# Optimization experiments

Hardware: AMD Instinct MI355X
Metric: run time of the kernel (lower is better)

The kernel has to match this reference:

```python
import jax, jax.numpy as jnp
import numpy as np

K = 5  # filter_size (matches init_kwargs)


def _adaptive_pool_matrix(size: int, k: int) -> jnp.ndarray:
    """Row-stochastic [k, size] matrix replicating torch adaptive_avg_pool1d bins."""
    P = np.zeros((k, size), np.float32)
    for i in range(k):
        s = (i * size) // k
        e = -((-(i + 1) * size) // k)  # ceil((i+1)*size/k)
        P[i, s:e] = 1.0 / (e - s)
    return jnp.asarray(P)


def setup_inputs() -> dict:
    key = jax.random.key(0)
    k1, k2, k3 = jax.random.split(key, 3)
    B, Cin, Cout, H, W = 8, 32, 32, 256, 256
    x = jax.random.normal(k1, (B, Cin, H, W), jnp.float32)
    conv_w = jax.random.normal(k2, (Cout, Cin), jnp.float32) * (1.0 / np.sqrt(Cin))
    conv_b = jax.random.normal(k3, (Cout,), jnp.float32) * 0.01
    return {"x": x, "conv_w": conv_w, "conv_b": conv_b}


def reference(x, conv_w, conv_b):
    B, Cin, H, W = x.shape
    # 1x1 conv == channel-mixing einsum
    feat = jnp.einsum('bihw,oi->bohw', x, conv_w) + conv_b[None, :, None, None]
    C = feat.shape[1]
    # adaptive_avg_pool2d(feat, K) via static pooling matrices -> per-(b,c) KxK filter
    Ph = _adaptive_pool_matrix(H, K)
    Pw = _adaptive_pool_matrix(W, K)
    filt = jnp.einsum('kh,bchw,lw->bckl', Ph, feat, Pw)  # [B, C, K, K]
    # pad per original intent ('same' output), then grouped conv with groups=B*C
    pad = (K - 1) // 2
    if (K - 1) % 2 == 0:
        p = ((pad, pad), (pad, pad))
    else:
        p = ((pad + 1, pad), (pad + 1, pad))
    inp = feat.reshape(1, B * C, H, W)
    w = filt.reshape(B * C, 1, K, K)
    out = jax.lax.conv_general_dilated(
        inp, w, window_strides=(1, 1), padding=p,
        dimension_numbers=('NCHW', 'OIHW', 'NCHW'),
        feature_group_count=B * C)
    return out.reshape(B, C, H, W)
```

## Files before the change

### kernel.cpp

```cpp
#include <hip/hip_runtime.h>
#include <hip/hip_bf16.h>


#define CIN 32
#define COUT 32
#define HW 256
#define PLANE (HW * HW)
#define BATCH 8
#define KF 5

__global__ __launch_bounds__(256) void conv1x1_kernel(const float* __restrict__ x,
                                                      const float* __restrict__ Wm,
                                                      const float* __restrict__ bias,
                                                      float* __restrict__ feat) {
    int b  = blockIdx.x >> 7;
    int hp = blockIdx.x & 127;
    int h0 = hp * 2;
    int w  = threadIdx.x;

    const float* xb = x + (size_t)b * CIN * PLANE + h0 * HW + w;
    float xv0[CIN], xv1[CIN];
#pragma unroll
    for (int i = 0; i < CIN; ++i) {
        xv0[i] = xb[i * PLANE];
        xv1[i] = xb[i * PLANE + HW];
    }
    float* fb = feat + (size_t)b * COUT * PLANE + h0 * HW + w;
#pragma unroll 4
    for (int o = 0; o < COUT; ++o) {
        float a0 = bias[o];
        float a1 = a0;
#pragma unroll
        for (int i = 0; i < CIN; ++i) {
            float wv = Wm[o * CIN + i];
            a0 += wv * xv0[i];
            a1 += wv * xv1[i];
        }
        fb[o * PLANE] = a0;
        fb[o * PLANE + HW] = a1;
    }
}

__global__ __launch_bounds__(256) void pool_kernel(const float* __restrict__ feat,
                                                   float* __restrict__ filt) {
    int bo = blockIdx.x / KF;
    int k  = blockIdx.x % KF;
    int sk = (k * HW) / KF;
    int ek = ((k + 1) * HW + KF - 1) / KF;
    int t  = threadIdx.x;

    const float* f = feat + (size_t)bo * PLANE + t;
    float cs = 0.f;
    for (int h = sk; h < ek; ++h) cs += f[h * HW];

    __shared__ float col[256];
    col[t] = cs;
    __syncthreads();

    if (t < KF) {
        int sl = (t * HW) / KF;
        int el = ((t + 1) * HW + KF - 1) / KF;
        float s = 0.f;
        for (int w2 = sl; w2 < el; ++w2) s += col[w2];
        filt[bo * (KF * KF) + k * KF + t] = s / (float)((ek - sk) * (el - sl));
    }
}

__global__ __launch_bounds__(256) void dwconv_kernel(const float* __restrict__ feat,
                                                     const float* __restrict__ filt,
                                                     float* __restrict__ out) {
    int bo   = blockIdx.y;
    int tile = blockIdx.x;
    int ty   = tile >> 3, tx_ = tile & 7;
    int oy0  = ty * 32, ox0 = tx_ * 32;

    __shared__ __align__(16) float s[36 * 36];
    __shared__ float sfilt[25];

    const float* fb = feat + (size_t)bo * PLANE;
    int t = threadIdx.x;
    if (t < 25) sfilt[t] = filt[bo * 25 + t];

    for (int idx = t; idx < 36 * 36; idx += 256) {
        int r = idx / 36;
        int c = idx - r * 36;
        int gy = oy0 - 2 + r;
        int gx = ox0 - 2 + c;
        float v = 0.f;
        if ((unsigned)gy < (unsigned)HW && (unsigned)gx < (unsigned)HW) v = fb[gy * HW + gx];
        s[c * 36 + r] = v;
    }
    __syncthreads();

    float f[25];
#pragma unroll
    for (int j = 0; j < 25; ++j) f[j] = sfilt[j];

    int tx = t & 31;
    int tq = t >> 5;
    float acc0 = 0.f, acc1 = 0.f, acc2 = 0.f, acc3 = 0.f;

#pragma unroll
    for (int kw = 0; kw < 5; ++kw) {
        const float* colp = &s[(tx + kw) * 36 + 4 * tq];
        float4 lo = *(const float4*)(colp);
        float4 hi = *(const float4*)(colp + 4);
        float r0 = lo.x, r1 = lo.y, r2 = lo.z, r3 = lo.w;
        float r4 = hi.x, r5 = hi.y, r6 = hi.z, r7 = hi.w;
#pragma unroll
        for (int kh = 0; kh < 5; ++kh) {
            float wv = f[kh * 5 + kw];
            float v0 = (kh == 0) ? r0 : (kh == 1) ? r1 : (kh == 2) ? r2 : (kh == 3) ? r3 : r4;
            float v1 = (kh == 0) ? r1 : (kh == 1) ? r2 : (kh == 2) ? r3 : (kh == 3) ? r4 : r5;
            float v2 = (kh == 0) ? r2 : (kh == 1) ? r3 : (kh == 2) ? r4 : (kh == 3) ? r5 : r6;
            float v3 = (kh == 0) ? r3 : (kh == 1) ? r4 : (kh == 2) ? r5 : (kh == 3) ? r6 : r7;
            acc0 += wv * v0;
            acc1 += wv * v1;
            acc2 += wv * v2;
            acc3 += wv * v3;
        }
    }

    float* ob = out + (size_t)bo * PLANE;
    int gx = ox0 + tx;
    int gy = oy0 + 4 * tq;
    ob[(gy + 0) * HW + gx] = acc0;
    ob[(gy + 1) * HW + gx] = acc1;
    ob[(gy + 2) * HW + gx] = acc2;
    ob[(gy + 3) * HW + gx] = acc3;
}

extern "C" void kernel_launch(void* const* d_in, const int* in_sizes, int n_in,
                              void* d_out, int out_size, void* d_ws, size_t ws_size,
                              hipStream_t stream) {
    const float* x      = (const float*)d_in[0];
    const float* conv_w = (const float*)d_in[1];
    const float* conv_b = (const float*)d_in[2];
    float* out = (float*)d_out;

    float* feat = (float*)d_ws;
    float* filt = feat + (size_t)BATCH * COUT * PLANE;

    conv1x1_kernel<<<dim3(BATCH * 128), dim3(256), 0, stream>>>(x, conv_w, conv_b, feat);
    pool_kernel<<<dim3(BATCH * COUT * KF), dim3(256), 0, stream>>>(feat, filt);
    dwconv_kernel<<<dim3(64, BATCH * COUT), dim3(256), 0, stream>>>(feat, filt, out);
}
```

Measured before the change: 190.5 us.

## Vectorize conv1x1 and pooling loads, restructure depthwise conv into full-width row strips

The 1x1 conv now has each thread handle four contiguous pixels with float4 loads and stores, using half as many blocks. The pooling kernel reads 4-row-interleaved float4 chunks and hardcodes the bin size of 52, which holds for a 256-wide plane split into 5 bins. The depthwise conv switches from 32x32 tiles to 32-row full-width strips with a sliding 5-row register window and float4 staging into LDS, which cuts halo overhead and LDS traffic. The trade-off is fewer blocks and more registers per thread in the conv kernels.

```diff
diff --git a/kernel.cpp b/kernel.cpp
--- a/kernel.cpp
+++ b/kernel.cpp
@@ -1,5 +1,4 @@
 #include <hip/hip_runtime.h>
-#include <hip/hip_bf16.h>
 
 
 #define CIN 32
@@ -8,36 +7,33 @@
 #define PLANE (HW * HW)
 #define BATCH 8
 #define KF 5
+#define BIN 52
 
 __global__ __launch_bounds__(256) void conv1x1_kernel(const float* __restrict__ x,
                                                       const float* __restrict__ Wm,
                                                       const float* __restrict__ bias,
                                                       float* __restrict__ feat) {
-    int b  = blockIdx.x >> 7;
-    int hp = blockIdx.x & 127;
-    int h0 = hp * 2;
-    int w  = threadIdx.x;
+    int b  = blockIdx.x >> 6;
+    int rg = blockIdx.x & 63;
+    int p0 = rg * 1024 + threadIdx.x * 4;
 
-    const float* xb = x + (size_t)b * CIN * PLANE + h0 * HW + w;
-    float xv0[CIN], xv1[CIN];
+    const float* xb = x + (size_t)b * CIN * PLANE + p0;
+    float4 xv[CIN];
 #pragma unroll
-    for (int i = 0; i < CIN; ++i) {
-        xv0[i] = xb[i * PLANE];
-        xv1[i] = xb[i * PLANE + HW];
-    }
-    float* fb = feat + (size_t)b * COUT * PLANE + h0 * HW + w;
+    for (int i = 0; i < CIN; ++i) xv[i] = *(const float4*)(xb + (size_t)i * PLANE);
+
+    float* fb = feat + (size_t)b * COUT * PLANE + p0;
 #pragma unroll 4
     for (int o = 0; o < COUT; ++o) {
-        float a0 = bias[o];
-        float a1 = a0;
+        float bv = bias[o];
+        float4 a; a.x = bv; a.y = bv; a.z = bv; a.w = bv;
 #pragma unroll
         for (int i = 0; i < CIN; ++i) {
             float wv = Wm[o * CIN + i];
-            a0 += wv * xv0[i];
-            a1 += wv * xv1[i];
+            a.x += wv * xv[i].x; a.y += wv * xv[i].y;
+            a.z += wv * xv[i].z; a.w += wv * xv[i].w;
         }
-        fb[o * PLANE] = a0;
-        fb[o * PLANE + HW] = a1;
+        *(float4*)(fb + (size_t)o * PLANE) = a;
     }
 }
 
@@ -46,88 +42,102 @@
     int bo = blockIdx.x / KF;
     int k  = blockIdx.x % KF;
     int sk = (k * HW) / KF;
-    int ek = ((k + 1) * HW + KF - 1) / KF;
     int t  = threadIdx.x;
+    int c4 = t & 63;
+    int rq = t >> 6;
 
-    const float* f = feat + (size_t)bo * PLANE + t;
-    float cs = 0.f;
-    for (int h = sk; h < ek; ++h) cs += f[h * HW];
+    const float* f = feat + (size_t)bo * PLANE + (sk + rq) * HW + c4 * 4;
+    float4 a = {0.f, 0.f, 0.f, 0.f};
+#pragma unroll
+    for (int j = 0; j < 13; ++j) {
+        float4 v = *(const float4*)(f + j * 4 * HW);
+        a.x += v.x; a.y += v.y; a.z += v.z; a.w += v.w;
+    }
 
-    __shared__ float col[256];
-    col[t] = cs;
+    __shared__ float4 red[256];
+    __shared__ float cols[256];
+    red[t] = a;
     __syncthreads();
-
+    if (t < 64) {
+        float4 r0 = red[t], r1 = red[t + 64], r2 = red[t + 128], r3 = red[t + 192];
+        cols[4 * t + 0] = r0.x + r1.x + r2.x + r3.x;
+        cols[4 * t + 1] = r0.y + r1.y + r2.y + r3.y;
+        cols[4 * t + 2] = r0.z + r1.z + r2.z + r3.z;
+        cols[4 * t + 3] = r0.w + r1.w + r2.w + r3.w;
+    }
+    __syncthreads();
     if (t < KF) {
         int sl = (t * HW) / KF;
-        int el = ((t + 1) * HW + KF - 1) / KF;
         float s = 0.f;
-        for (int w2 = sl; w2 < el; ++w2) s += col[w2];
-        filt[bo * (KF * KF) + k * KF + t] = s / (float)((ek - sk) * (el - sl));
+        for (int w = 0; w < BIN; ++w) s += cols[sl + w];
+        filt[bo * 25 + k * KF + t] = s * (1.0f / (BIN * BIN));
     }
 }
 
+#define LROW 264
 __global__ __launch_bounds__(256) void dwconv_kernel(const float* __restrict__ feat,
                                                      const float* __restrict__ filt,
                                                      float* __restrict__ out) {
-    int bo   = blockIdx.y;
-    int tile = blockIdx.x;
-    int ty   = tile >> 3, tx_ = tile & 7;
-    int oy0  = ty * 32, ox0 = tx_ * 32;
+    int bo    = blockIdx.y;
+    int strip = blockIdx.x;
+    int gy0   = strip * 32;
+    int t     = threadIdx.x;
 
-    __shared__ __align__(16) float s[36 * 36];
+    __shared__ __align__(16) float s[36 * LROW];
     __shared__ float sfilt[25];
+    if (t < 25) sfilt[t] = filt[bo * 25 + t];
+    if (t < 144) {
+        int lr = t >> 2, e = t & 3;
+        int ci = (e < 2) ? (2 + e) : (258 + e);
+        s[lr * LROW + ci] = 0.f;
+    }
 
     const float* fb = feat + (size_t)bo * PLANE;
-    int t = threadIdx.x;
-    if (t < 25) sfilt[t] = filt[bo * 25 + t];
-
-    for (int idx = t; idx < 36 * 36; idx += 256) {
-        int r = idx / 36;
-        int c = idx - r * 36;
-        int gy = oy0 - 2 + r;
-        int gx = ox0 - 2 + c;
-        float v = 0.f;
-        if ((unsigned)gy < (unsigned)HW && (unsigned)gx < (unsigned)HW) v = fb[gy * HW + gx];
-        s[c * 36 + r] = v;
+#pragma unroll
+    for (int j = 0; j < 9; ++j) {
+        int idx = t + 256 * j;
+        int lr  = idx >> 6;
+        int cx  = (idx & 63) * 4;
+        int gy  = gy0 - 2 + lr;
+        float4 v = {0.f, 0.f, 0.f, 0.f};
+        if ((unsigned)gy < (unsigned)HW) v = *(const float4*)(fb + gy * HW + cx);
+        *(float4*)(&s[lr * LROW + 4 + cx]) = v;
     }
     __syncthreads();
 
-    float f[25];
+    float fw[25];
 #pragma unroll
-    for (int j = 0; j < 25; ++j) f[j] = sfilt[j];
+    for (int j = 0; j < 25; ++j) fw[j] = sfilt[j];
 
-    int tx = t & 31;
-    int tq = t >> 5;
-    float acc0 = 0.f, acc1 = 0.f, acc2 = 0.f, acc3 = 0.f;
-
+    int c = t;
+    float w0[5], w1[5], w2[5], w3[5], w4[5];
 #pragma unroll
-    for (int kw = 0; kw < 5; ++kw) {
-        const float* colp = &s[(tx + kw) * 36 + 4 * tq];
-        float4 lo = *(const float4*)(colp);
-        float4 hi = *(const float4*)(colp + 4);
-        float r0 = lo.x, r1 = lo.y, r2 = lo.z, r3 = lo.w;
-        float r4 = hi.x, r5 = hi.y, r6 = hi.z, r7 = hi.w;
+    for (int j = 0; j < 5; ++j) {
+        w0[j] = s[0 * LROW + 2 + c + j];
+        w1[j] = s[1 * LROW + 2 + c + j];
+        w2[j] = s[2 * LROW + 2 + c + j];
+        w3[j] = s[3 * LROW + 2 + c + j];
+    }
+    float* ob = out + (size_t)bo * PLANE + (size_t)gy0 * HW + c;
 #pragma unroll
-        for (int kh = 0; kh < 5; ++kh) {
-            float wv = f[kh * 5 + kw];
-            float v0 = (kh == 0) ? r0 : (kh == 1) ? r1 : (kh == 2) ? r2 : (kh == 3) ? r3 : r4;
-            float v1 = (kh == 0) ? r1 : (kh == 1) ? r2 : (kh == 2) ? r3 : (kh == 3) ? r4 : r5;
-            float v2 = (kh == 0) ? r2 : (kh == 1) ? r3 : (kh == 2) ? r4 : (kh == 3) ? r5 : r6;
-            float v3 = (kh == 0) ? r3 : (kh == 1) ? r4 : (kh == 2) ? r5 : (kh == 3) ? r6 : r7;
-            acc0 += wv * v0;
-            acc1 += wv * v1;
-            acc2 += wv * v2;
-            acc3 += wv * v3;
+    for (int r = 0; r < 32; ++r) {
+#pragma unroll
+        for (int j = 0; j < 5; ++j) w4[j] = s[(r + 4) * LROW + 2 + c + j];
+        float acc = 0.f;
+#pragma unroll
+        for (int j = 0; j < 5; ++j) {
+            acc += fw[0 * 5 + j] * w0[j];
+            acc += fw[1 * 5 + j] * w1[j];
+            acc += fw[2 * 5 + j] * w2[j];
+            acc += fw[3 * 5 + j] * w3[j];
+            acc += fw[4 * 5 + j] * w4[j];
+        }
+        ob[r * HW] = acc;
+#pragma unroll
+        for (int j = 0; j < 5; ++j) {
+            w0[j] = w1[j]; w1[j] = w2[j]; w2[j] = w3[j]; w3[j] = w4[j];
         }
     }
-
-    float* ob = out + (size_t)bo * PLANE;
-    int gx = ox0 + tx;
-    int gy = oy0 + 4 * tq;
-    ob[(gy + 0) * HW + gx] = acc0;
-    ob[(gy + 1) * HW + gx] = acc1;
-    ob[(gy + 2) * HW + gx] = acc2;
-    ob[(gy + 3) * HW + gx] = acc3;
 }
 
 extern "C" void kernel_launch(void* const* d_in, const int* in_sizes, int n_in,
@@ -141,7 +151,7 @@
     float* feat = (float*)d_ws;
     float* filt = feat + (size_t)BATCH * COUT * PLANE;
 
-    conv1x1_kernel<<<dim3(BATCH * 128), dim3(256), 0, stream>>>(x, conv_w, conv_b, feat);
+    conv1x1_kernel<<<dim3(BATCH * 64), dim3(256), 0, stream>>>(x, conv_w, conv_b, feat);
     pool_kernel<<<dim3(BATCH * COUT * KF), dim3(256), 0, stream>>>(feat, filt);
-    dwconv_kernel<<<dim3(64, BATCH * COUT), dim3(256), 0, stream>>>(feat, filt, out);
+    dwconv_kernel<<<dim3(8, BATCH * COUT), dim3(256), 0, stream>>>(feat, filt, out);
 }
```

New measurement: 188.7 us. Within noise of the previous version (-0.9%).
